# Performance work log

Hardware: AMD Instinct MI355X
Metric: run time of the kernel (lower is better)

## Reference

```python
import jax, jax.numpy as jnp
import numpy as np

EPS = 1e-6


def setup_inputs() -> dict:
    key = jax.random.key(0)
    x = jax.random.normal(key, (64, 256, 64, 64), dtype=jnp.float32)
    return {"x": x}


def reference(x):
    # x: (B, C, H, W)
    B, C, H, W = x.shape
    N = H * W
    # --- covariance pooling ---
    xr = x.reshape(B, C, N)                       # (B, C, N)
    xc = xr - xr.mean(axis=2, keepdims=True)      # mean-center over spatial
    cov = jnp.einsum('bcn,bdn->bcd', xc, xc) / (N - 1)  # (B, C, C)
    # --- matrix square root via eigh ---
    eigvals, eigvecs = jnp.linalg.eigh(cov)       # (B, C), (B, C, C)
    sqrt_eigvals = jnp.sqrt(jnp.clip(eigvals, EPS, None))
    # V diag(sqrt(w)) V^T without materializing diag
    sqrt_mat = jnp.einsum('bic,bc,bjc->bij', eigvecs, sqrt_eigvals, eigvecs)
    # --- upper-triangular vectorization (incl. diagonal) ---
    row_idx, col_idx = jnp.triu_indices(C)
    return sqrt_mat[:, row_idx, col_idx]          # (B, C*(C+1)//2)
```

## Files before the change

kernel.cpp:

```cpp
#include <hip/hip_runtime.h>
#include <hip/hip_bf16.h>
#include <math.h>


#define B_ 64
#define C_ 256
#define N_ 4096
#define TRI ((C_*(C_+1))/2)
#define MATE (C_*C_)
#define TOTE ((size_t)B_*MATE)
#define KS 4
#define KW (N_/KS)

typedef __attribute__((ext_vector_type(8))) short bf16x8;
typedef __attribute__((ext_vector_type(4))) short short4v;
typedef __attribute__((ext_vector_type(4))) float f32x4;

__device__ __forceinline__ short f2bf(float f) {
    unsigned u = __float_as_uint(f);
    return (short)((u + 0x7FFFu + ((u >> 16) & 1u)) >> 16);
}
__device__ __forceinline__ float bf2f(short s) {
    return __uint_as_float(((unsigned)(unsigned short)s) << 16);
}
__device__ __forceinline__ void gload_lds16(const void* g, void* l) {
    __builtin_amdgcn_global_load_lds(
        (const __attribute__((address_space(1))) void*)g,
        (__attribute__((address_space(3))) void*)l, 16, 0, 0);
}
__device__ __forceinline__ bf16x8 ds_read16s(unsigned addr) {
    bf16x8 r;
    asm volatile("ds_read_b128 %0, %1" : "=v"(r) : "v"(addr));
    return r;
}
__device__ __forceinline__ void lgkm0_fence() {
    asm volatile("s_waitcnt lgkmcnt(0)" ::: "memory");
    __builtin_amdgcn_sched_barrier(0);
}

__global__ __launch_bounds__(256) void convert_sums(const float* __restrict__ x,
                                                    short* __restrict__ xb,
                                                    float* __restrict__ S) {
    int row = blockIdx.x;
    const float* p = x + (size_t)row * N_;
    short* q = xb + (size_t)row * N_;
    int tid = threadIdx.x;
    float s = 0.f;
    #pragma unroll
    for (int i = 0; i < 2; ++i) {
        int e = (tid + i * 256) * 8;
        f32x4 u = *(const f32x4*)(p + e);
        f32x4 v = *(const f32x4*)(p + e + 4);
        s += u[0] + u[1] + u[2] + u[3] + v[0] + v[1] + v[2] + v[3];
        bf16x8 o;
        #pragma unroll
        for (int k = 0; k < 4; ++k) { o[k] = f2bf(u[k]); o[4 + k] = f2bf(v[k]); }
        *(bf16x8*)(q + e) = o;
    }
    for (int off = 32; off; off >>= 1) s += __shfl_down(s, off);
    __shared__ float red[4];
    if ((tid & 63) == 0) red[tid >> 6] = s;
    __syncthreads();
    if (tid == 0) S[row] = red[0] + red[1] + red[2] + red[3];
}

__global__ __launch_bounds__(1024) void gram_cov(const short* __restrict__ xb,
                                                 short* __restrict__ Gp) {
    int bid = (blockIdx.x & 7) * 32 + (blockIdx.x >> 3);
    int b = bid >> 2, slab = bid & 3;
    const char* xs = (const char*)(xb + (size_t)b * C_ * N_ + (size_t)slab * KW);

    __shared__ short Xs[2][32768];

    int tid = threadIdx.x;
    int lane = tid & 63, wid = tid >> 6;
    int wr = wid >> 2, wc = wid & 3;
    int lr = lane & 15, hi = lane >> 4;

    unsigned xs0 = (unsigned)(unsigned long long)
        (__attribute__((address_space(3))) char*)&Xs[0][0];
    unsigned swz = (unsigned)((lr & 7) << 4);
    unsigned rowA = (unsigned)((wr * 64 + lr) * 256);
    unsigned rowB = (unsigned)((wc * 64 + lr) * 256);

    f32x4 acc[4][4] = {};

    #pragma unroll
    for (int q = 0; q < 4; ++q) {
        int d = (q * 1024 + tid) * 16;
        int row = d >> 8;
        int inner = (d & 255) ^ ((row & 7) << 4);
        gload_lds16(xs + (size_t)row * (N_ * 2) + inner, (char*)Xs[0] + d);
    }
    __syncthreads();

    const int NSTEP = KW / 128;
    for (int c = 0; c < NSTEP; ++c) {
        if (c + 1 < NSTEP) {
            #pragma unroll
            for (int q = 0; q < 4; ++q) {
                int d = (q * 1024 + tid) * 16;
                int row = d >> 8;
                int inner = (d & 255) ^ ((row & 7) << 4);
                gload_lds16(xs + (size_t)row * (N_ * 2) + (c + 1) * 256 + inner,
                            (char*)Xs[(c + 1) & 1] + d);
            }
        }
        unsigned xsb = xs0 + (unsigned)((c & 1) * 65536);
        #pragma unroll
        for (int ks2 = 0; ks2 < 4; ++ks2) {
            unsigned o1 = ((unsigned)(ks2 * 64 + hi * 16)) ^ swz;
            bf16x8 af[4], bb[4];
            #pragma unroll
            for (int m = 0; m < 4; ++m)
                af[m] = ds_read16s(xsb + rowA + (unsigned)(m * 4096) + o1);
            #pragma unroll
            for (int n = 0; n < 4; ++n)
                bb[n] = ds_read16s(xsb + rowB + (unsigned)(n * 4096) + o1);
            lgkm0_fence();
            #pragma unroll
            for (int m = 0; m < 4; ++m)
                #pragma unroll
                for (int n = 0; n < 4; ++n)
                    acc[m][n] = __builtin_amdgcn_mfma_f32_16x16x32_bf16(af[m], bb[n], acc[m][n], 0, 0, 0);
        }
        __syncthreads();
    }

    short* G = Gp + ((size_t)slab * B_ + b) * MATE;
    #pragma unroll
    for (int m = 0; m < 4; ++m)
        #pragma unroll
        for (int n = 0; n < 4; ++n)
            #pragma unroll
            for (int r = 0; r < 4; ++r) {
                int i = wr * 64 + m * 16 + hi * 4 + r;
                int j = wc * 64 + n * 16 + lr;
                G[(size_t)i * C_ + j] = f2bf(acc[m][n][r]);
            }
}

__global__ __launch_bounds__(256) void trace_kernel(const short* __restrict__ Gp,
                                                    const float* __restrict__ S,
                                                    float* __restrict__ mArr) {
    int b = blockIdx.x, i = threadIdx.x;
    float s = S[b * C_ + i], g = 0.f;
    #pragma unroll
    for (int sl = 0; sl < KS; ++sl)
        g += bf2f(Gp[((size_t)sl * B_ + b) * MATE + (size_t)i * (C_ + 1)]);
    float c = (g - s * s * (1.0f / N_)) * (1.0f / (N_ - 1));
    __shared__ float red[256];
    red[i] = c;
    __syncthreads();
    for (int off = 128; off; off >>= 1) {
        if (i < off) red[i] += red[i + off];
        __syncthreads();
    }
    if (i == 0) {
        float m = red[0] * (1.0f / C_);
        mArr[b] = m;
        mArr[64 + b] = 1.0f / m;
        mArr[128 + b] = sqrtf(m);
    }
}

__global__ __launch_bounds__(256) void init_kernel(const short* __restrict__ Gp,
                                                   const float* __restrict__ S,
                                                   const float* __restrict__ mArr,
                                                   short* __restrict__ Y0,
                                                   short* __restrict__ Z1) {
    int idx = blockIdx.x * 256 + threadIdx.x;
    size_t e0 = (size_t)idx * 8;
    int b = (int)(e0 >> 16);
    int ij = (int)(e0 & 65535);
    int i = ij >> 8, j0 = ij & 255;
    float g[8] = {};
    #pragma unroll
    for (int sl = 0; sl < KS; ++sl) {
        bf16x8 t = *(const bf16x8*)(Gp + (size_t)sl * TOTE + e0);
        #pragma unroll
        for (int q = 0; q < 8; ++q) g[q] += bf2f(t[q]);
    }
    float Si = S[b * C_ + i];
    f32x4 sjA = *(const f32x4*)(S + b * C_ + j0);
    f32x4 sjB = *(const f32x4*)(S + b * C_ + j0 + 4);
    float invm = mArr[64 + b];
    const float invN = 1.0f / (float)N_;
    const float invN1 = 1.0f / (float)(N_ - 1);
    bf16x8 y, z;
    #pragma unroll
    for (int q = 0; q < 8; ++q) {
        float sj = (q < 4) ? sjA[q] : sjB[q - 4];
        float cov = (g[q] - Si * sj * invN) * invN1;
        float a = cov * invm;
        y[q] = f2bf(a);
        z[q] = f2bf(((i == j0 + q) ? 1.5f : 0.0f) - 0.5f * a);
    }
    *(bf16x8*)(Y0 + e0) = y;
    *(bf16x8*)(Z1 + e0) = z;
}

template<int EP, bool DUAL>
__global__ __launch_bounds__(256) void ns_gemm(
        const short* A0, const short* B0, const short* Ba0, void* C0,
        const short* A1, const short* B1, const short* Ba1, void* C1,
        const float* __restrict__ mArr) {
    int nb = gridDim.x, per = nb >> 3;
    int bid = (blockIdx.x & 7) * per + (blockIdx.x >> 3);
    const short *A = A0, *B = B0, *Ba = Ba0; void* C = C0;
    if (DUAL && bid >= (nb >> 1)) { bid -= nb >> 1; A = A1; B = B1; Ba = Ba1; C = C1; }
    int b, ti, tj;
    if constexpr (EP == 2) {
        b = bid / 3; int t = bid % 3;
        ti = (t == 2) ? 1 : 0; tj = (t == 0) ? 0 : 1;
    } else {
        b = bid >> 2; int t = bid & 3;
        ti = t >> 1; tj = t & 1;
    }
    const short* Ap = A + (size_t)b * MATE + (size_t)ti * 128 * C_;
    const short* Bp = B + (size_t)b * MATE + (size_t)tj * 128 * C_;

    __shared__ short As[16384], Bs[16384];

    int tid = threadIdx.x, lane = tid & 63, wid = tid >> 6;
    int wr = wid >> 1, wc = wid & 1;
    int lr = lane & 15, hi = lane >> 4;
    f32x4 acc[4][4] = {};

    for (int h = 0; h < 2; ++h) {
        #pragma unroll
        for (int q = 0; q < 8; ++q) {
            int d = (q * 256 + tid) * 16;
            int row = d >> 8;
            int inner = (d & 255) ^ ((row & 7) << 4);
            gload_lds16((const char*)Ap + (size_t)row * 512 + h * 256 + inner,
                        (char*)As + d);
            gload_lds16((const char*)Bp + (size_t)row * 512 + h * 256 + inner,
                        (char*)Bs + d);
        }
        __syncthreads();
        #pragma unroll
        for (int ks = 0; ks < 4; ++ks) {
            bf16x8 af[4], bb[4];
            #pragma unroll
            for (int m = 0; m < 4; ++m) {
                int rowa = wr * 64 + m * 16 + lr;
                af[m] = *(const bf16x8*)((const char*)As + rowa * 256 +
                                         ((ks * 64 + hi * 16) ^ ((rowa & 7) << 4)));
                int rowb = wc * 64 + m * 16 + lr;
                bb[m] = *(const bf16x8*)((const char*)Bs + rowb * 256 +
                                         ((ks * 64 + hi * 16) ^ ((rowb & 7) << 4)));
            }
            #pragma unroll
            for (int m = 0; m < 4; ++m)
                #pragma unroll
                for (int n = 0; n < 4; ++n)
                    acc[m][n] = __builtin_amdgcn_mfma_f32_16x16x32_bf16(af[m], bb[n], acc[m][n], 0, 0, 0);
        }
        if (h == 0) __syncthreads();
    }

    int r0 = hi * 4;
    float sqm = (EP == 2) ? mArr[128 + b] : 0.f;
    #pragma unroll
    for (int m = 0; m < 4; ++m)
        #pragma unroll
        for (int n = 0; n < 4; ++n)
            #pragma unroll
            for (int r = 0; r < 4; ++r) {
                int i = ti * 128 + wr * 64 + m * 16 + r0 + r;
                int j = tj * 128 + wc * 64 + n * 16 + lr;
                size_t idx = (size_t)b * MATE + (size_t)i * C_ + j;
                float v = acc[m][n][r];
                if constexpr (EP == 0) {
                    ((short*)C)[idx] = f2bf(v);
                } else if constexpr (EP == 1) {
                    ((short*)C)[idx] = f2bf(1.5f * bf2f(Ba[idx]) - 0.5f * v);
                } else {
                    if (j >= i) {
                        size_t o = (size_t)b * TRI + (size_t)i * C_ - (size_t)(i * (i - 1)) / 2 + (j - i);
                        ((float*)C)[o] = sqm * (1.5f * bf2f(Ba[idx]) - 0.5f * v);
                    }
                }
            }
}

extern "C" void kernel_launch(void* const* d_in, const int* in_sizes, int n_in,
                              void* d_out, int out_size, void* d_ws, size_t ws_size,
                              hipStream_t stream) {
    const float* x = (const float*)d_in[0];
    float* out = (float*)d_out;

    float* mArr = (float*)d_ws;
    float* S    = mArr + 256;
    short* Gp   = (short*)(S + 16384);
    short* xbuf = Gp + (size_t)KS * TOTE;
    short* bufs = xbuf + (size_t)B_ * C_ * N_;
    short* M0 = bufs;
    short* M1 = bufs + TOTE;
    short* M2 = bufs + 2 * TOTE;
    short* M3 = bufs + 3 * TOTE;
    short* M4 = bufs + 4 * TOTE;

    convert_sums<<<B_ * C_, 256, 0, stream>>>(x, xbuf, S);
    gram_cov<<<B_ * KS, 1024, 0, stream>>>(xbuf, Gp);
    trace_kernel<<<B_, 256, 0, stream>>>(Gp, S, mArr);
    init_kernel<<<(int)(TOTE / 8 / 256), 256, 0, stream>>>(Gp, S, mArr, M0, M1);

    ns_gemm<1, false><<<256, 256, 0, stream>>>(M0, M0, M0, M2,
                                               nullptr, nullptr, nullptr, nullptr, nullptr);
    ns_gemm<0, false><<<256, 256, 0, stream>>>(M1, M2, nullptr, M3,
                                               nullptr, nullptr, nullptr, nullptr, nullptr);
    ns_gemm<1, true><<<512, 256, 0, stream>>>(M2, M3, M2, M4,
                                              M3, M1, M1, M0, nullptr);
    ns_gemm<0, false><<<256, 256, 0, stream>>>(M0, M4, nullptr, M2,
                                               nullptr, nullptr, nullptr, nullptr, nullptr);
    ns_gemm<2, false><<<B_ * 3, 256, 0, stream>>>(M4, M2, M4, out,
                                                  nullptr, nullptr, nullptr, nullptr, mArr);
}
```

Baseline: 194.4 us.

## Store bf16 input in chunk-tiled layout for contiguous Gram tile loads

The conversion kernel now writes the bf16 copy of x in a blocked layout of [batch, slab, chunk, channel, 128], so that each 256-channel by 128-element tile the Gram kernel loads sits in one contiguous 64 KB block. The Gram kernel's global-to-LDS loads then read contiguous memory instead of rows strided by the full spatial length. The conversion kernel is also restructured so each block handles 8 channels, with 32 lanes per channel and a 32-wide shuffle reduction. The scattered 16-byte writes in the conversion kernel may be less coalesced than before.

```diff
diff --git a/kernel.cpp b/kernel.cpp
--- a/kernel.cpp
+++ b/kernel.cpp
@@ -11,6 +11,7 @@
 #define TOTE ((size_t)B_*MATE)
 #define KS 4
 #define KW (N_/KS)
+#define NCH 8
 
 typedef __attribute__((ext_vector_type(8))) short bf16x8;
 typedef __attribute__((ext_vector_type(4))) short short4v;
@@ -39,36 +40,43 @@
 }
 
 __global__ __launch_bounds__(256) void convert_sums(const float* __restrict__ x,
-                                                    short* __restrict__ xb,
+                                                    short* __restrict__ xb2,
                                                     float* __restrict__ S) {
-    int row = blockIdx.x;
-    const float* p = x + (size_t)row * N_;
-    short* q = xb + (size_t)row * N_;
+    int bid = blockIdx.x;
+    int b = bid >> 5;
+    int c0 = (bid & 31) * 8;
     int tid = threadIdx.x;
+    int cl = tid >> 5;
+    int ln = tid & 31;
+    int c = c0 + cl;
+    const float* px = x + ((size_t)(b * C_ + c)) * N_;
     float s = 0.f;
     #pragma unroll
-    for (int i = 0; i < 2; ++i) {
-        int e = (tid + i * 256) * 8;
-        f32x4 u = *(const f32x4*)(p + e);
-        f32x4 v = *(const f32x4*)(p + e + 4);
+    for (int st = 0; st < 16; ++st) {
+        int p = ln + st * 32;
+        int slab = p >> 7, chunk = (p >> 4) & 7, piece = p & 15;
+        f32x4 u = *(const f32x4*)(px + p * 8);
+        f32x4 v = *(const f32x4*)(px + p * 8 + 4);
         s += u[0] + u[1] + u[2] + u[3] + v[0] + v[1] + v[2] + v[3];
         bf16x8 o;
         #pragma unroll
         for (int k = 0; k < 4; ++k) { o[k] = f2bf(u[k]); o[4 + k] = f2bf(v[k]); }
-        *(bf16x8*)(q + e) = o;
-    }
-    for (int off = 32; off; off >>= 1) s += __shfl_down(s, off);
-    __shared__ float red[4];
-    if ((tid & 63) == 0) red[tid >> 6] = s;
-    __syncthreads();
-    if (tid == 0) S[row] = red[0] + red[1] + red[2] + red[3];
-}
-
-__global__ __launch_bounds__(1024) void gram_cov(const short* __restrict__ xb,
+        size_t e = ((((size_t)(b * KS + slab) * NCH + chunk) * C_ + c) * 128) + piece * 8;
+        *(bf16x8*)(xb2 + e) = o;
+    }
+    s += __shfl_down(s, 16, 32);
+    s += __shfl_down(s, 8, 32);
+    s += __shfl_down(s, 4, 32);
+    s += __shfl_down(s, 2, 32);
+    s += __shfl_down(s, 1, 32);
+    if (ln == 0) S[b * C_ + c] = s;
+}
+
+__global__ __launch_bounds__(1024) void gram_cov(const short* __restrict__ xb2,
                                                  short* __restrict__ Gp) {
     int bid = (blockIdx.x & 7) * 32 + (blockIdx.x >> 3);
     int b = bid >> 2, slab = bid & 3;
-    const char* xs = (const char*)(xb + (size_t)b * C_ * N_ + (size_t)slab * KW);
+    const char* xs = (const char*)(xb2 + (size_t)(b * KS + slab) * NCH * C_ * 128);
 
     __shared__ short Xs[2][32768];
 
@@ -89,20 +97,19 @@
     for (int q = 0; q < 4; ++q) {
         int d = (q * 1024 + tid) * 16;
         int row = d >> 8;
-        int inner = (d & 255) ^ ((row & 7) << 4);
-        gload_lds16(xs + (size_t)row * (N_ * 2) + inner, (char*)Xs[0] + d);
+        int src = (d & ~255) | ((d & 255) ^ ((row & 7) << 4));
+        gload_lds16(xs + src, (char*)Xs[0] + d);
     }
     __syncthreads();
 
-    const int NSTEP = KW / 128;
-    for (int c = 0; c < NSTEP; ++c) {
-        if (c + 1 < NSTEP) {
+    for (int c = 0; c < NCH; ++c) {
+        if (c + 1 < NCH) {
             #pragma unroll
             for (int q = 0; q < 4; ++q) {
                 int d = (q * 1024 + tid) * 16;
                 int row = d >> 8;
-                int inner = (d & 255) ^ ((row & 7) << 4);
-                gload_lds16(xs + (size_t)row * (N_ * 2) + (c + 1) * 256 + inner,
+                int src = (d & ~255) | ((d & 255) ^ ((row & 7) << 4));
+                gload_lds16(xs + (c + 1) * 65536 + src,
                             (char*)Xs[(c + 1) & 1] + d);
             }
         }
@@ -302,7 +309,7 @@
     short* M3 = bufs + 3 * TOTE;
     short* M4 = bufs + 4 * TOTE;
 
-    convert_sums<<<B_ * C_, 256, 0, stream>>>(x, xbuf, S);
+    convert_sums<<<B_ * C_ / 8, 256, 0, stream>>>(x, xbuf, S);
     gram_cov<<<B_ * KS, 1024, 0, stream>>>(xbuf, Gp);
     trace_kernel<<<B_, 256, 0, stream>>>(Gp, S, mArr);
     init_kernel<<<(int)(TOTE / 8 / 256), 256, 0, stream>>>(Gp, S, mArr, M0, M1);
```

Result: no change. 197.1 us (+1.4%).
